# Kernel optimization log

Measured on AMD Instinct MI355X. Metric: run time of the kernel, lower is better.

## Reference

```python
import jax, jax.numpy as jnp
import numpy as np

B, S, D = 2, 2048, 1024
H, HD = 16, 64
ROPE_BASE = 1000.0


def rope(x):
    # x: [B, H, S, hd]; interleaved (GPT-NeoX-style pairs) rotary embedding, base=1000
    d = x.shape[-1]
    theta = 1.0 / (ROPE_BASE ** (jnp.arange(0, d, 2, dtype=jnp.float32) / d))  # [d/2]
    theta = jnp.repeat(theta, 2)                                               # [d]
    pos = jnp.arange(x.shape[-2], dtype=jnp.float32)                           # [S]
    pm = pos[:, None] * theta[None, :]                                         # [S, d]
    cos, sin = jnp.cos(pm), jnp.sin(pm)
    # rotated: _x[..., 0::2] = -x[..., 1::2]; _x[..., 1::2] = x[..., 0::2]
    rot = jnp.stack([-x[..., 1::2], x[..., 0::2]], axis=-1).reshape(x.shape)
    return x * cos + rot * sin


def setup_inputs() -> dict:
    key = jax.random.key(0)
    ks = jax.random.split(key, 12)
    sc = 1.0 / np.sqrt(D)
    inp = {
        "query": jax.random.normal(ks[0], (B, S, D), jnp.float32),
        "key": jax.random.normal(ks[1], (B, S, D), jnp.float32),
        "value": jax.random.normal(ks[2], (B, S, D), jnp.float32),
        "mask": jnp.broadcast_to(jnp.tril(jnp.ones((S, S), jnp.int32)), (B, S, S)),
        "Wq": jax.random.normal(ks[3], (D, H * HD), jnp.float32) * sc,
        "bq": jax.random.normal(ks[4], (H * HD,), jnp.float32) * 0.01,
        "Wk": jax.random.normal(ks[5], (D, H * HD), jnp.float32) * sc,
        "bk": jax.random.normal(ks[6], (H * HD,), jnp.float32) * 0.01,
        "Wv": jax.random.normal(ks[7], (D, H * HD), jnp.float32) * sc,
        "bv": jax.random.normal(ks[8], (H * HD,), jnp.float32) * 0.01,
        "Wo": jax.random.normal(ks[9], (H * HD, D), jnp.float32) * sc,
        "bo": jax.random.normal(ks[10], (D,), jnp.float32) * 0.01,
    }
    return inp


def reference(query, key, value, mask, Wq, bq, Wk, bk, Wv, bv, Wo, bo):
    b = query.shape[0]
    split = lambda t: t.reshape(b, -1, H, HD).transpose(0, 2, 1, 3)  # [B,H,S,hd]
    q = split(query @ Wq + bq)
    k = split(key @ Wk + bk)
    v = split(value @ Wv + bv)
    qr, kr = rope(q), rope(k)
    scale = jnp.sqrt(jnp.float32(HD))
    num = jnp.exp(jnp.einsum("bhqd,bhkd->bhqk", qr, kr) / scale)           # [B,H,S,S]
    den = jnp.sum(jnp.exp(jnp.einsum("bhqd,bhkd->bhqk", q, k) / scale),
                  axis=-1, keepdims=True)                                   # [B,H,S,1]
    a = num / den
    a = jnp.where(mask[:, None, :, :] == 0, -jnp.inf, a)
    alpha = jax.nn.softmax(a, axis=-1)
    z = jnp.einsum("bhqk,bhkd->bhqd", alpha, v)
    z = z.transpose(0, 2, 1, 3).reshape(b, -1, H * HD)
    return z @ Wo + bo
```

## Files before the change

kernel.cpp:

```cpp
#include <hip/hip_runtime.h>


#define Bn 2
#define Sn 2048
#define Dn 1024
#define Hn 16
#define HDn 64

typedef __attribute__((ext_vector_type(8))) short bf16x8;
typedef __attribute__((ext_vector_type(8))) unsigned short u16x8;
typedef __attribute__((ext_vector_type(4))) unsigned short u16x4;
typedef __attribute__((ext_vector_type(4))) float f32x4;
typedef uint2 __attribute__((may_alias)) uint2a;
typedef float __attribute__((may_alias)) floata;

#define MFMA(a, b, c) __builtin_amdgcn_mfma_f32_16x16x32_bf16(a, b, c, 0, 0, 0)
#define Z4 ((f32x4){0.f, 0.f, 0.f, 0.f})

#define PRESC 0.18033688011112042f
#define C2 0.5287663729448977f

#define EXP2(x) __builtin_amdgcn_exp2f(x)
#define LOG2(x) __builtin_amdgcn_logf(x)

__device__ __forceinline__ unsigned short f2bf(float f) {
  unsigned int u = __builtin_bit_cast(unsigned int, f);
  u = (u + 0x7fffu + ((u >> 16) & 1u)) >> 16;
  return (unsigned short)u;
}
__device__ __forceinline__ float bf2f(unsigned short u) {
  return __builtin_bit_cast(float, (unsigned int)u << 16);
}

__device__ __forceinline__ unsigned int cvtpk(float lo, float hi) {
  unsigned int r;
  asm("v_cvt_pk_bf16_f32 %0, %1, %2" : "=v"(r) : "v"(lo), "v"(hi));
  return r;
}

__device__ __forceinline__ void gll16(const unsigned short* g, unsigned short* l) {
  __builtin_amdgcn_global_load_lds((const __attribute__((address_space(1))) void*)g,
                                   (__attribute__((address_space(3))) void*)l, 16, 0, 0);
}

#define FR(T, row, x) (*(const bf16x8*)&(T)[(row) * 64 + (((x) ^ ((row) & 7)) * 8)])

__global__ __launch_bounds__(256) void k_pre(
    const float* __restrict__ W0, const float* __restrict__ W1,
    const float* __restrict__ W2, const float* __restrict__ W3,
    unsigned short* __restrict__ O0, unsigned short* __restrict__ O1,
    unsigned short* __restrict__ O2, unsigned short* __restrict__ O3,
    const float* __restrict__ qa, const float* __restrict__ ka, const float* __restrict__ va,
    unsigned short* __restrict__ oq, unsigned short* __restrict__ ok,
    unsigned short* __restrict__ ov, float2* __restrict__ T) {
  __shared__ float t[64][65];
  const int b = blockIdx.x;
  const int tid = threadIdx.x;
  if (b < 256) {
    const int idx = b * 256 + tid;
    const int s = idx >> 5, i = idx & 31;
    const float theta = powf(1000.f, -(float)i / 32.f);
    const float pm = (float)s * theta;
    T[idx] = make_float2(cosf(pm), sinf(pm));
  } else if (b < 1280) {
    const int w = b - 256;
    const int which = w >> 8, rem = w & 255;
    const float* W = (which == 0) ? W0 : (which == 1) ? W1 : (which == 2) ? W2 : W3;
    unsigned short* O = (which == 0) ? O0 : (which == 1) ? O1 : (which == 2) ? O2 : O3;
    const int kb = (rem >> 4) * 64, nb = (rem & 15) * 64;
#pragma unroll
    for (int rep = 0; rep < 16; ++rep) {
      const int e = rep * 256 + tid;
      const int k = e >> 6, n = e & 63;
      t[k][n] = W[(kb + k) * Dn + nb + n];
    }
    __syncthreads();
#pragma unroll
    for (int rep = 0; rep < 16; ++rep) {
      const int e = rep * 256 + tid;
      const int n = e >> 6, k = e & 63;
      O[(nb + n) * Dn + kb + k] = f2bf(t[k][n]);
    }
  } else {
    const int c = b - 1280;
    const int z = c >> 11, cx = c & 2047;
    const float* s = (z == 0) ? qa : (z == 1) ? ka : va;
    unsigned short* d = (z == 0) ? oq : (z == 1) ? ok : ov;
    const size_t idx = ((size_t)cx * 256 + tid) * 8;
    float4 a0 = *(const float4*)(s + idx);
    float4 b0 = *(const float4*)(s + idx + 4);
    u16x8 pk;
    pk[0] = f2bf(a0.x); pk[1] = f2bf(a0.y); pk[2] = f2bf(a0.z); pk[3] = f2bf(a0.w);
    pk[4] = f2bf(b0.x); pk[5] = f2bf(b0.y); pk[6] = f2bf(b0.z); pk[7] = f2bf(b0.w);
    *(u16x8*)(d + idx) = pk;
  }
}

__global__ __launch_bounds__(256) void k_gemm_proj(
    const unsigned short* __restrict__ Qa, const unsigned short* __restrict__ Ka,
    const unsigned short* __restrict__ Va,
    const unsigned short* __restrict__ Wq, const unsigned short* __restrict__ Wk,
    const unsigned short* __restrict__ Wv,
    const float* __restrict__ bqp, const float* __restrict__ bkp, const float* __restrict__ bvp,
    const float2* __restrict__ trig,
    unsigned short* __restrict__ Qb, unsigned short* __restrict__ Kb,
    unsigned short* __restrict__ Qr, unsigned short* __restrict__ Kr,
    unsigned short* __restrict__ Vt) {
  __shared__ unsigned short SH[17408];
  unsigned short* Al = SH;
  unsigned short* Bl = SH + 8192;
  const int tid = threadIdx.x;
  const int wave = tid >> 6, lane = tid & 63, g = lane >> 4, li = lane & 15;
  const int mbase = blockIdx.x * 128, nbase = blockIdx.y * 128;
  const int wm = wave >> 1, wn = wave & 1;
  const int which = blockIdx.z;
  const unsigned short* A = (which == 0) ? Qa : (which == 1) ? Ka : Va;
  const unsigned short* Wt = (which == 0) ? Wq : (which == 1) ? Wk : Wv;
  const float* bias = (which == 0) ? bqp : (which == 1) ? bkp : bvp;

  f32x4 acc[4][4];
#pragma unroll
  for (int i = 0; i < 4; ++i)
#pragma unroll
    for (int j = 0; j < 4; ++j) acc[i][j] = Z4;

  float bv4[4];
#pragma unroll
  for (int nt = 0; nt < 4; ++nt) bv4[nt] = bias[nbase + wn * 64 + nt * 16 + li];

  const int lr8 = lane >> 3, lc = lane & 7;
  const int xc8 = (lc ^ lr8) * 8;
  const unsigned short* srcA = A + (size_t)(mbase + wave * 32 + lr8) * Dn + xc8;
  const unsigned short* srcB = Wt + (size_t)(nbase + wave * 32 + lr8) * Dn + xc8;

  for (int kb = 0; kb < Dn; kb += 64) {
    __syncthreads();
#pragma unroll
    for (int i = 0; i < 4; ++i) {
      gll16(srcA + kb + (size_t)i * (8 * Dn), &Al[(wave * 32 + i * 8) * 64]);
      gll16(srcB + kb + (size_t)i * (8 * Dn), &Bl[(wave * 32 + i * 8) * 64]);
    }
    __syncthreads();
#pragma unroll
    for (int kc = 0; kc < 2; ++kc) {
      bf16x8 af[4], bfr[4];
#pragma unroll
      for (int mt = 0; mt < 4; ++mt) af[mt] = FR(Al, wm * 64 + mt * 16 + li, kc * 4 + g);
#pragma unroll
      for (int nt = 0; nt < 4; ++nt) bfr[nt] = FR(Bl, wn * 64 + nt * 16 + li, kc * 4 + g);
#pragma unroll
      for (int mt = 0; mt < 4; ++mt)
#pragma unroll
        for (int nt = 0; nt < 4; ++nt)
          acc[mt][nt] = MFMA(af[mt], bfr[nt], acc[mt][nt]);
    }
  }

  if (which < 2) {
    unsigned short* Ob = (which == 0) ? Qb : Kb;
    unsigned short* Or = (which == 0) ? Qr : Kr;
    const float presc = (which == 0) ? PRESC : 1.f;
    __syncthreads();
#pragma unroll
    for (int mt = 0; mt < 4; ++mt)
#pragma unroll
      for (int nt = 0; nt < 4; ++nt) {
        const int nl = wn * 64 + nt * 16 + li;
#pragma unroll
        for (int r = 0; r < 4; ++r) {
          const int ml = wm * 64 + mt * 16 + 4 * g + r;
          SH[ml * 136 + nl] = f2bf((acc[mt][nt][r] + bv4[nt]) * presc);
        }
      }
    __syncthreads();
#pragma unroll
    for (int hp = 0; hp < 2; ++hp) {
#pragma unroll
      for (int pass = 0; pass < 4; ++pass) {
        const int row = pass * 32 + wave * 8 + (lane >> 3);
        const int nl = hp * 64 + (lane & 7) * 8;
        const int mg = mbase + row;
        const int bi = mg >> 11, sg = mg & (Sn - 1);
        const int ng = nbase + nl;
        const int h = ng >> 6, hd = ng & 63;
        const u16x8 v = *(const u16x8*)&SH[row * 136 + nl];
        u16x8 o;
        const float2* tp = trig + (sg << 5) + (hd >> 1);
#pragma unroll
        for (int j = 0; j < 4; ++j) {
          const float x0 = bf2f(v[2 * j]), x1 = bf2f(v[2 * j + 1]);
          const float2 cs = tp[j];
          o[2 * j] = f2bf(x0 * cs.x - x1 * cs.y);
          o[2 * j + 1] = f2bf(x1 * cs.x + x0 * cs.y);
        }
        const size_t oi = (((size_t)(bi * Hn + h)) * Sn + sg) * HDn + hd;
        *(u16x8*)(Ob + oi) = v;
        *(u16x8*)(Or + oi) = o;
      }
    }
  } else {
#pragma unroll
    for (int mt = 0; mt < 4; ++mt) {
#pragma unroll
      for (int nt = 0; nt < 4; ++nt) {
        const int n = nbase + wn * 64 + nt * 16 + li;
        const int h = n >> 6, hd = n & 63;
        const int m0 = mbase + wm * 64 + mt * 16 + 4 * g;
        const int b = m0 >> 11, s0 = m0 & (Sn - 1);
        u16x4 pk;
#pragma unroll
        for (int r = 0; r < 4; ++r) pk[r] = f2bf(acc[mt][nt][r] + bv4[nt]);
        *(u16x4*)&Vt[(((size_t)(b * Hn + h)) * HDn + hd) * Sn + s0] = pk;
      }
    }
  }
}

__global__ __launch_bounds__(256) void k_gemm_out(const unsigned short* __restrict__ A,
                                                  const unsigned short* __restrict__ Wt,
                                                  const float* __restrict__ bias,
                                                  float* __restrict__ out) {
  __shared__ unsigned short Al[64 * 64];
  __shared__ unsigned short Bl[128 * 64];
  const int tid = threadIdx.x;
  const int wave = tid >> 6, lane = tid & 63, g = lane >> 4, li = lane & 15;
  const int mbase = blockIdx.x * 64, nbase = blockIdx.y * 128;
  const int wm = wave >> 1, wn = wave & 1;

  f32x4 acc[2][4];
#pragma unroll
  for (int i = 0; i < 2; ++i)
#pragma unroll
    for (int j = 0; j < 4; ++j) acc[i][j] = Z4;

  float bv4[4];
#pragma unroll
  for (int nt = 0; nt < 4; ++nt) bv4[nt] = bias[nbase + wn * 64 + nt * 16 + li];

  const int lr8 = lane >> 3, lc = lane & 7;
  const int xc8 = (lc ^ lr8) * 8;
  const unsigned short* srcA = A + (size_t)(mbase + wave * 16 + lr8) * Dn + xc8;
  const unsigned short* srcB = Wt + (size_t)(nbase + wave * 32 + lr8) * Dn + xc8;

  for (int kb = 0; kb < Dn; kb += 64) {
    __syncthreads();
#pragma unroll
    for (int i = 0; i < 2; ++i)
      gll16(srcA + kb + (size_t)i * (8 * Dn), &Al[(wave * 16 + i * 8) * 64]);
#pragma unroll
    for (int i = 0; i < 4; ++i)
      gll16(srcB + kb + (size_t)i * (8 * Dn), &Bl[(wave * 32 + i * 8) * 64]);
    __syncthreads();
#pragma unroll
    for (int kc = 0; kc < 2; ++kc) {
      bf16x8 af[2], bfr[4];
#pragma unroll
      for (int mt = 0; mt < 2; ++mt) af[mt] = FR(Al, wm * 32 + mt * 16 + li, kc * 4 + g);
#pragma unroll
      for (int nt = 0; nt < 4; ++nt) bfr[nt] = FR(Bl, wn * 64 + nt * 16 + li, kc * 4 + g);
#pragma unroll
      for (int mt = 0; mt < 2; ++mt)
#pragma unroll
        for (int nt = 0; nt < 4; ++nt)
          acc[mt][nt] = MFMA(af[mt], bfr[nt], acc[mt][nt]);
    }
  }

#pragma unroll
  for (int mt = 0; mt < 2; ++mt)
#pragma unroll
    for (int nt = 0; nt < 4; ++nt) {
      const int n = nbase + wn * 64 + nt * 16 + li;
#pragma unroll
      for (int r = 0; r < 4; ++r) {
        const int m = mbase + wm * 32 + mt * 16 + 4 * g + r;
        out[(size_t)m * Dn + n] = acc[mt][nt][r] + bv4[nt];
      }
    }
}

__global__ __launch_bounds__(256, 4) void k_attn(
    const unsigned short* __restrict__ Qr, const unsigned short* __restrict__ Kr,
    const unsigned short* __restrict__ Qb, const unsigned short* __restrict__ Kb,
    const unsigned short* __restrict__ Vt, unsigned short* __restrict__ Zb) {
  __shared__ unsigned short KT[2][8192];
  __shared__ unsigned short Pl[4][1024];

  const int tid = threadIdx.x;
  const int wave = tid >> 6, lane = tid & 63, g = lane >> 4, li = lane & 15;
  const int bid = blockIdx.x;
  const int x = bid & 7, m = bid >> 3;
  const int Qd = m >> 5, wv = m & 31, v = wv & 7;
  const int bh = x * 4 + (wv >> 3);
  const int qt = (Qd == 0) ? v : (Qd == 1) ? 15 - v : (Qd == 2) ? 16 + v : 31 - v;
  const int q0 = qt * 64;
  const int qw = q0 + wave * 16;
  const size_t kvbase = (size_t)bh * (Sn * HDn);

  const int lr8 = lane >> 3, lc = lane & 7;
  const int xc8 = (lc ^ lr8) * 8;

  bf16x8 qbfA[4][2];
#pragma unroll
  for (int jq = 0; jq < 4; ++jq)
#pragma unroll
    for (int kc = 0; kc < 2; ++kc)
      qbfA[jq][kc] =
          *(const bf16x8*)(Qb + kvbase + (size_t)(q0 + jq * 16 + li) * HDn + kc * 32 + g * 8);

  const unsigned short* srcPA = Kb + kvbase + (size_t)(wave * 32 + lr8) * HDn + xc8;
  const int tw = wave >> 1, rbB = (wave & 1) * 32;
  const unsigned short* srcKrB = Kr + kvbase + (size_t)(rbB + lr8) * HDn + xc8;
  const unsigned short* srcVtB = Vt + kvbase + (size_t)(rbB + lr8) * Sn + xc8;
  const size_t strIB = tw ? (size_t)(8 * Sn) : (size_t)(8 * HDn);
  unsigned short* myP = &Pl[wave][0];

  bool dm[4];
#pragma unroll
  for (int r = 0; r < 4; ++r) dm[r] = (4 * g + r) <= li;

#define STAGE_PA(kb_, buf_)                                 \
  do {                                                      \
    unsigned short* d_ = &KT[buf_][(wave * 32) * 64];       \
    const unsigned short* s_ = srcPA + (size_t)(kb_)*HDn;   \
    gll16(s_, d_);                                          \
    gll16(s_ + 8 * HDn, d_ + 8 * 64);                       \
    gll16(s_ + 16 * HDn, d_ + 16 * 64);                     \
    gll16(s_ + 24 * HDn, d_ + 24 * 64);                     \
  } while (0)

#define STAGE_B(kb_, buf_)                                                    \
  do {                                                                        \
    unsigned short* d_ = &KT[buf_][tw * 4096 + rbB * 64];                     \
    const unsigned short* s_ =                                                \
        tw ? (srcVtB + (size_t)(kb_)) : (srcKrB + (size_t)(kb_)*HDn);         \
    gll16(s_, d_);                                                            \
    gll16(s_ + strIB, d_ + 8 * 64);                                           \
    gll16(s_ + 2 * strIB, d_ + 16 * 64);                                      \
    gll16(s_ + 3 * strIB, d_ + 24 * 64);                                      \
  } while (0)

  float dacc[4][4];
#pragma unroll
  for (int jq = 0; jq < 4; ++jq)
#pragma unroll
    for (int r = 0; r < 4; ++r) dacc[jq][r] = 0.f;

  STAGE_PA(0, 0);
  __syncthreads();
  for (int t = 0; t < Sn / 128; ++t) {
    if (t + 1 < Sn / 128) STAGE_PA((t + 1) * 128, (t + 1) & 1);
    const unsigned short* TK = &KT[t & 1][0];
#pragma unroll
    for (int sub = 0; sub < 2; ++sub) {
      const int krow = wave * 32 + sub * 16 + li;
      const bf16x8 kf0 = FR(TK, krow, g), kf1 = FR(TK, krow, 4 + g);
      f32x4 s[4];
#pragma unroll
      for (int jq = 0; jq < 4; ++jq) {
        s[jq] = MFMA(kf0, qbfA[jq][0], Z4);
        s[jq] = MFMA(kf1, qbfA[jq][1], s[jq]);
      }
#pragma unroll
      for (int jq = 0; jq < 4; ++jq)
#pragma unroll
        for (int r = 0; r < 4; ++r) dacc[jq][r] += EXP2(s[jq][r]);
    }
    __syncthreads();
  }

  floata* Dred = (floata*)&Pl[0][0];
#pragma unroll
  for (int jq = 0; jq < 4; ++jq) {
    float pd = (dacc[jq][0] + dacc[jq][1]) + (dacc[jq][2] + dacc[jq][3]);
    pd += __shfl_xor(pd, 16);
    pd += __shfl_xor(pd, 32);
    if (lane < 16) Dred[wave * 64 + jq * 16 + li] = pd;
  }
  __syncthreads();
  const float den = (Dred[0 * 64 + wave * 16 + li] + Dred[1 * 64 + wave * 16 + li]) +
                    (Dred[2 * 64 + wave * 16 + li] + Dred[3 * 64 + wave * 16 + li]);
  const float Lc = LOG2(den) - C2;
  const f32x4 mLc = {-Lc, -Lc, -Lc, -Lc};

  bf16x8 qrf[2];
#pragma unroll
  for (int kc = 0; kc < 2; ++kc)
    qrf[kc] = *(const bf16x8*)(Qr + kvbase + (size_t)(qw + li) * HDn + kc * 32 + g * 8);

  f32x4 accz[4];
#pragma unroll
  for (int i = 0; i < 4; ++i) accz[i] = Z4;
  float ws[4] = {0.f, 0.f, 0.f, 0.f};
  const int NTB = qt + 1;

  STAGE_B(0, 0);
  __syncthreads();
  for (int t = 0; t < NTB; ++t) {
    if (t + 1 < NTB) STAGE_B((t + 1) * 64, (t + 1) & 1);
    const unsigned short* T0 = &KT[t & 1][0];
    const unsigned short* TV = &KT[t & 1][0] + 4096;
    const bool last = (t == qt);
#pragma unroll
    for (int nt = 0; nt < 4; ++nt) {
      float w4[4];
      if (!last || nt <= wave) {
        const int krow = nt * 16 + li;
        const bf16x8 kf0 = FR(T0, krow, g), kf1 = FR(T0, krow, 4 + g);
        f32x4 s = mLc;
        s = MFMA(kf0, qrf[0], s);
        s = MFMA(kf1, qrf[1], s);
        if (last && nt == wave) {
#pragma unroll
          for (int r = 0; r < 4; ++r) {
            const float e = EXP2(EXP2(s[r]));
            w4[r] = dm[r] ? e : 0.f;
            ws[r] += w4[r];
          }
        } else {
#pragma unroll
          for (int r = 0; r < 4; ++r) {
            w4[r] = EXP2(EXP2(s[r]));
            ws[r] += w4[r];
          }
        }
      } else {
        w4[0] = w4[1] = w4[2] = w4[3] = 0.f;
      }
      const int adr = li * 64 + (((nt * 2 + (g >> 1)) ^ (li & 7)) * 8) + (g & 1) * 4;
      *(uint2a*)&myP[adr] = (uint2a){cvtpk(w4[0], w4[1]), cvtpk(w4[2], w4[3])};
    }
    __builtin_amdgcn_sched_barrier(0);
#pragma unroll
    for (int kc = 0; kc < 2; ++kc) {
      const bf16x8 pa = FR(myP, li, kc * 4 + g);
#pragma unroll
      for (int n2 = 0; n2 < 4; ++n2) {
        const bf16x8 vb = FR(TV, n2 * 16 + li, kc * 4 + g);
        accz[n2] = MFMA(pa, vb, accz[n2]);
      }
    }
    __syncthreads();
  }

  float wsum = (ws[0] + ws[1]) + (ws[2] + ws[3]);
  wsum += __shfl_xor(wsum, 16);
  wsum += __shfl_xor(wsum, 32);
  float rw[4];
#pragma unroll
  for (int r = 0; r < 4; ++r) rw[r] = 1.f / __shfl(wsum, 4 * g + r);
  const int b = bh >> 4, h = bh & 15;
#pragma unroll
  for (int n2 = 0; n2 < 4; ++n2) {
#pragma unroll
    for (int r = 0; r < 4; ++r) {
      const int hd = n2 * 16 + li;
      const int q = qw + 4 * g + r;
      Zb[((size_t)(b * Sn + q)) * Dn + h * HDn + hd] = f2bf(accz[n2][r] * rw[r]);
    }
  }
#undef STAGE_PA
#undef STAGE_B
}

extern "C" void kernel_launch(void* const* d_in, const int* in_sizes, int n_in,
                              void* d_out, int out_size, void* d_ws, size_t ws_size,
                              hipStream_t stream) {
  const float* query = (const float*)d_in[0];
  const float* key   = (const float*)d_in[1];
  const float* value = (const float*)d_in[2];
  const float* Wq = (const float*)d_in[4];
  const float* bq = (const float*)d_in[5];
  const float* Wk = (const float*)d_in[6];
  const float* bk = (const float*)d_in[7];
  const float* Wv = (const float*)d_in[8];
  const float* bv = (const float*)d_in[9];
  const float* Wo = (const float*)d_in[10];
  const float* bo = (const float*)d_in[11];

  char* ws = (char*)d_ws;
  const size_t MB = 1ull << 20;
  unsigned short* Wqt = (unsigned short*)(ws + 0 * MB);
  unsigned short* Wkt = (unsigned short*)(ws + 2 * MB);
  unsigned short* Wvt = (unsigned short*)(ws + 4 * MB);
  unsigned short* Wot = (unsigned short*)(ws + 6 * MB);
  float2* trig        = (float2*)(ws + 8 * MB);
  unsigned short* Qa  = (unsigned short*)(ws + 9 * MB);
  unsigned short* Ka  = (unsigned short*)(ws + 17 * MB);
  unsigned short* Va  = (unsigned short*)(ws + 25 * MB);
  unsigned short* Qb  = (unsigned short*)(ws + 33 * MB);
  unsigned short* Kb  = (unsigned short*)(ws + 41 * MB);
  unsigned short* Qr  = (unsigned short*)(ws + 49 * MB);
  unsigned short* Kr  = (unsigned short*)(ws + 57 * MB);
  unsigned short* Vt  = (unsigned short*)(ws + 65 * MB);
  unsigned short* Zb  = (unsigned short*)(ws + 73 * MB);

  k_pre<<<7424, 256, 0, stream>>>(Wq, Wk, Wv, Wo, Wqt, Wkt, Wvt, Wot,
                                  query, key, value, Qa, Ka, Va, trig);
  k_gemm_proj<<<dim3(32, 8, 3), 256, 0, stream>>>(Qa, Ka, Va, Wqt, Wkt, Wvt,
                                                  bq, bk, bv, trig, Qb, Kb, Qr, Kr, Vt);
  k_attn<<<1024, 256, 0, stream>>>(Qr, Kr, Qb, Kb, Vt, Zb);
  k_gemm_out<<<dim3(64, 8), 256, 0, stream>>>(Zb, Wot, bo, (float*)d_out);
}
```

Before: 135.2 us.

## Pair causal low/high query tiles in 512-thread attention blocks to share K/V staging

```diff
diff --git a/kernel.cpp b/kernel.cpp
--- a/kernel.cpp
+++ b/kernel.cpp
@@ -279,39 +279,41 @@
     }
 }
 
-__global__ __launch_bounds__(256, 4) void k_attn(
+__global__ __launch_bounds__(512, 4) void k_attn(
     const unsigned short* __restrict__ Qr, const unsigned short* __restrict__ Kr,
     const unsigned short* __restrict__ Qb, const unsigned short* __restrict__ Kb,
     const unsigned short* __restrict__ Vt, unsigned short* __restrict__ Zb) {
   __shared__ unsigned short KT[2][8192];
-  __shared__ unsigned short Pl[4][1024];
+  __shared__ unsigned short Pl[8][1024];
 
   const int tid = threadIdx.x;
   const int wave = tid >> 6, lane = tid & 63, g = lane >> 4, li = lane & 15;
+  const int wl = wave & 3, half = wave >> 2;
   const int bid = blockIdx.x;
   const int x = bid & 7, m = bid >> 3;
-  const int Qd = m >> 5, wv = m & 31, v = wv & 7;
-  const int bh = x * 4 + (wv >> 3);
-  const int qt = (Qd == 0) ? v : (Qd == 1) ? 15 - v : (Qd == 2) ? 16 + v : 31 - v;
-  const int q0 = qt * 64;
-  const int qw = q0 + wave * 16;
+  const int bh = x * 4 + (m & 3);
+  const int f = m >> 2;
+  const int tL = f, tH = 31 - f;
+  const int qt_w = half ? tH : tL;
+  const int qw = qt_w * 64 + wl * 16;
   const size_t kvbase = (size_t)bh * (Sn * HDn);
 
   const int lr8 = lane >> 3, lc = lane & 7;
   const int xc8 = (lc ^ lr8) * 8;
 
-  bf16x8 qbfA[4][2];
-#pragma unroll
-  for (int jq = 0; jq < 4; ++jq)
+  bf16x8 qbfA[8][2];
+#pragma unroll
+  for (int jq = 0; jq < 8; ++jq) {
+    const int qrow = ((jq < 4) ? tL : tH) * 64 + (jq & 3) * 16 + li;
 #pragma unroll
     for (int kc = 0; kc < 2; ++kc)
-      qbfA[jq][kc] =
-          *(const bf16x8*)(Qb + kvbase + (size_t)(q0 + jq * 16 + li) * HDn + kc * 32 + g * 8);
-
-  const unsigned short* srcPA = Kb + kvbase + (size_t)(wave * 32 + lr8) * HDn + xc8;
-  const int tw = wave >> 1, rbB = (wave & 1) * 32;
-  const unsigned short* srcKrB = Kr + kvbase + (size_t)(rbB + lr8) * HDn + xc8;
-  const unsigned short* srcVtB = Vt + kvbase + (size_t)(rbB + lr8) * Sn + xc8;
+      qbfA[jq][kc] = *(const bf16x8*)(Qb + kvbase + (size_t)qrow * HDn + kc * 32 + g * 8);
+  }
+
+  const unsigned short* srcPA = Kb + kvbase + (size_t)(wave * 16 + lr8) * HDn + xc8;
+  const int tw = half;
+  const unsigned short* srcKrB = Kr + kvbase + (size_t)(wl * 16 + lr8) * HDn + xc8;
+  const unsigned short* srcVtB = Vt + kvbase + (size_t)(wl * 16 + lr8) * Sn + xc8;
   const size_t strIB = tw ? (size_t)(8 * Sn) : (size_t)(8 * HDn);
   unsigned short* myP = &Pl[wave][0];
 
@@ -321,28 +323,24 @@
 
 #define STAGE_PA(kb_, buf_)                                 \
   do {                                                      \
-    unsigned short* d_ = &KT[buf_][(wave * 32) * 64];       \
+    unsigned short* d_ = &KT[buf_][(wave * 16) * 64];       \
     const unsigned short* s_ = srcPA + (size_t)(kb_)*HDn;   \
     gll16(s_, d_);                                          \
     gll16(s_ + 8 * HDn, d_ + 8 * 64);                       \
-    gll16(s_ + 16 * HDn, d_ + 16 * 64);                     \
-    gll16(s_ + 24 * HDn, d_ + 24 * 64);                     \
   } while (0)
 
 #define STAGE_B(kb_, buf_)                                                    \
   do {                                                                        \
-    unsigned short* d_ = &KT[buf_][tw * 4096 + rbB * 64];                     \
+    unsigned short* d_ = &KT[buf_][tw * 4096 + (wl * 16) * 64];               \
     const unsigned short* s_ =                                                \
         tw ? (srcVtB + (size_t)(kb_)) : (srcKrB + (size_t)(kb_)*HDn);         \
     gll16(s_, d_);                                                            \
-    gll16(s_ + strIB, d_ + 8 * 64);                                           \
-    gll16(s_ + 2 * strIB, d_ + 16 * 64);                                      \
-    gll16(s_ + 3 * strIB, d_ + 24 * 64);                                      \
+    gll16(s_ + strIB, d_ + 8 * 64);                                          \
   } while (0)
 
-  float dacc[4][4];
-#pragma unroll
-  for (int jq = 0; jq < 4; ++jq)
+  float dacc[8][4];
+#pragma unroll
+  for (int jq = 0; jq < 8; ++jq)
 #pragma unroll
     for (int r = 0; r < 4; ++r) dacc[jq][r] = 0.f;
 
@@ -351,35 +349,30 @@
   for (int t = 0; t < Sn / 128; ++t) {
     if (t + 1 < Sn / 128) STAGE_PA((t + 1) * 128, (t + 1) & 1);
     const unsigned short* TK = &KT[t & 1][0];
-#pragma unroll
-    for (int sub = 0; sub < 2; ++sub) {
-      const int krow = wave * 32 + sub * 16 + li;
-      const bf16x8 kf0 = FR(TK, krow, g), kf1 = FR(TK, krow, 4 + g);
-      f32x4 s[4];
-#pragma unroll
-      for (int jq = 0; jq < 4; ++jq) {
-        s[jq] = MFMA(kf0, qbfA[jq][0], Z4);
-        s[jq] = MFMA(kf1, qbfA[jq][1], s[jq]);
-      }
-#pragma unroll
-      for (int jq = 0; jq < 4; ++jq)
-#pragma unroll
-        for (int r = 0; r < 4; ++r) dacc[jq][r] += EXP2(s[jq][r]);
+    const int krow = wave * 16 + li;
+    const bf16x8 kf0 = FR(TK, krow, g), kf1 = FR(TK, krow, 4 + g);
+#pragma unroll
+    for (int jq = 0; jq < 8; ++jq) {
+      f32x4 s = MFMA(kf0, qbfA[jq][0], Z4);
+      s = MFMA(kf1, qbfA[jq][1], s);
+#pragma unroll
+      for (int r = 0; r < 4; ++r) dacc[jq][r] += EXP2(s[r]);
     }
     __syncthreads();
   }
 
   floata* Dred = (floata*)&Pl[0][0];
 #pragma unroll
-  for (int jq = 0; jq < 4; ++jq) {
+  for (int jq = 0; jq < 8; ++jq) {
     float pd = (dacc[jq][0] + dacc[jq][1]) + (dacc[jq][2] + dacc[jq][3]);
     pd += __shfl_xor(pd, 16);
     pd += __shfl_xor(pd, 32);
-    if (lane < 16) Dred[wave * 64 + jq * 16 + li] = pd;
+    if (lane < 16) Dred[wave * 128 + jq * 16 + li] = pd;
   }
   __syncthreads();
-  const float den = (Dred[0 * 64 + wave * 16 + li] + Dred[1 * 64 + wave * 16 + li]) +
-                    (Dred[2 * 64 + wave * 16 + li] + Dred[3 * 64 + wave * 16 + li]);
+  float den = 0.f;
+#pragma unroll
+  for (int wp = 0; wp < 8; ++wp) den += Dred[wp * 128 + wave * 16 + li];
   const float Lc = LOG2(den) - C2;
   const f32x4 mLc = {-Lc, -Lc, -Lc, -Lc};
 
@@ -392,7 +385,7 @@
 #pragma unroll
   for (int i = 0; i < 4; ++i) accz[i] = Z4;
   float ws[4] = {0.f, 0.f, 0.f, 0.f};
-  const int NTB = qt + 1;
+  const int NTB = tH + 1;
 
   STAGE_B(0, 0);
   __syncthreads();
@@ -400,44 +393,46 @@
     if (t + 1 < NTB) STAGE_B((t + 1) * 64, (t + 1) & 1);
     const unsigned short* T0 = &KT[t & 1][0];
     const unsigned short* TV = &KT[t & 1][0] + 4096;
-    const bool last = (t == qt);
-#pragma unroll
-    for (int nt = 0; nt < 4; ++nt) {
-      float w4[4];
-      if (!last || nt <= wave) {
-        const int krow = nt * 16 + li;
-        const bf16x8 kf0 = FR(T0, krow, g), kf1 = FR(T0, krow, 4 + g);
-        f32x4 s = mLc;
-        s = MFMA(kf0, qrf[0], s);
-        s = MFMA(kf1, qrf[1], s);
-        if (last && nt == wave) {
-#pragma unroll
-          for (int r = 0; r < 4; ++r) {
-            const float e = EXP2(EXP2(s[r]));
-            w4[r] = dm[r] ? e : 0.f;
-            ws[r] += w4[r];
+    if (t <= qt_w) {
+      const bool last = (t == qt_w);
+#pragma unroll
+      for (int nt = 0; nt < 4; ++nt) {
+        float w4[4];
+        if (!last || nt <= wl) {
+          const int krow = nt * 16 + li;
+          const bf16x8 kf0 = FR(T0, krow, g), kf1 = FR(T0, krow, 4 + g);
+          f32x4 s = mLc;
+          s = MFMA(kf0, qrf[0], s);
+          s = MFMA(kf1, qrf[1], s);
+          if (last && nt == wl) {
+#pragma unroll
+            for (int r = 0; r < 4; ++r) {
+              const float e = EXP2(EXP2(s[r]));
+              w4[r] = dm[r] ? e : 0.f;
+              ws[r] += w4[r];
+            }
+          } else {
+#pragma unroll
+            for (int r = 0; r < 4; ++r) {
+              w4[r] = EXP2(EXP2(s[r]));
+              ws[r] += w4[r];
+            }
           }
         } else {
-#pragma unroll
-          for (int r = 0; r < 4; ++r) {
-            w4[r] = EXP2(EXP2(s[r]));
-            ws[r] += w4[r];
-          }
+          w4[0] = w4[1] = w4[2] = w4[3] = 0.f;
         }
-      } else {
-        w4[0] = w4[1] = w4[2] = w4[3] = 0.f;
-      }
-      const int adr = li * 64 + (((nt * 2 + (g >> 1)) ^ (li & 7)) * 8) + (g & 1) * 4;
-      *(uint2a*)&myP[adr] = (uint2a){cvtpk(w4[0], w4[1]), cvtpk(w4[2], w4[3])};
-    }
-    __builtin_amdgcn_sched_barrier(0);
-#pragma unroll
-    for (int kc = 0; kc < 2; ++kc) {
-      const bf16x8 pa = FR(myP, li, kc * 4 + g);
-#pragma unroll
-      for (int n2 = 0; n2 < 4; ++n2) {
-        const bf16x8 vb = FR(TV, n2 * 16 + li, kc * 4 + g);
-        accz[n2] = MFMA(pa, vb, accz[n2]);
+        const int adr = li * 64 + (((nt * 2 + (g >> 1)) ^ (li & 7)) * 8) + (g & 1) * 4;
+        *(uint2a*)&myP[adr] = (uint2a){cvtpk(w4[0], w4[1]), cvtpk(w4[2], w4[3])};
+      }
+      __builtin_amdgcn_sched_barrier(0);
+#pragma unroll
+      for (int kc = 0; kc < 2; ++kc) {
+        const bf16x8 pa = FR(myP, li, kc * 4 + g);
+#pragma unroll
+        for (int n2 = 0; n2 < 4; ++n2) {
+          const bf16x8 vb = FR(TV, n2 * 16 + li, kc * 4 + g);
+          accz[n2] = MFMA(pa, vb, accz[n2]);
+        }
       }
     }
     __syncthreads();
@@ -499,6 +494,6 @@
                                   query, key, value, Qa, Ka, Va, trig);
   k_gemm_proj<<<dim3(32, 8, 3), 256, 0, stream>>>(Qa, Ka, Va, Wqt, Wkt, Wvt,
                                                   bq, bk, bv, trig, Qb, Kb, Qr, Kr, Vt);
-  k_attn<<<1024, 256, 0, stream>>>(Qr, Kr, Qb, Kb, Vt, Zb);
+  k_attn<<<512, 512, 0, stream>>>(Qr, Kr, Qb, Kb, Vt, Zb);
   k_gemm_out<<<dim3(64, 8), 256, 0, stream>>>(Zb, Wot, bo, (float*)d_out);
 }
```

New measurement: 341.9 us. +152.9%, slower.
